# Kernel optimization log

Measured on AMD Instinct MI355X. Metric: run time of the kernel, lower is better.

## Reference

```python
import jax, jax.numpy as jnp
import numpy as np
import math

B, H, S, D = 4, 16, 4096, 128

def setup_inputs() -> dict:
    key = jax.random.key(0)
    kq, kk, kv = jax.random.split(key, 3)
    q = jax.random.normal(kq, (B, H, S, D), dtype=jnp.float32)
    k = jax.random.normal(kk, (B, H, S, D), dtype=jnp.float32)
    v = jax.random.normal(kv, (B, H, S, D), dtype=jnp.float32)
    return {"q": q, "k": k, "v": v}

def reference(q, k, v):
    # Faithful to the torch module: score = (q^T @ k) / sqrt(n_heads)
    # q^T contracts over the SEQUENCE axis -> (B, H, D, D) feature-attention.
    n_heads = q.shape[1]
    scale = 1.0 / math.sqrt(n_heads)
    score = jnp.einsum('bhsd,bhse->bhde', q, k) * scale  # (B,H,D,D)
    score = jax.nn.softmax(score, axis=-1)
    # score @ v^T -> (B,H,D,S)
    out = jnp.einsum('bhde,bhse->bhds', score, v)
    return out
```

## Files before the change

kernel.cpp:

```cpp
#include <hip/hip_runtime.h>

#define BH 64
#define S_ 4096
#define D_ 128
#define SCALE 0.25f

typedef __attribute__((ext_vector_type(4))) short short4v;
typedef __attribute__((ext_vector_type(8))) short short8v;
typedef __attribute__((ext_vector_type(4))) float f32x4;

__device__ inline unsigned short f2bf(float x) {
  union { float f; unsigned u; } v; v.f = x;
  unsigned r = v.u + 0x7fff + ((v.u >> 16) & 1);
  return (unsigned short)(r >> 16);
}
__device__ inline short8v cat8(short4v a, short4v b) {
  short8v r;
  r[0] = a[0]; r[1] = a[1]; r[2] = a[2]; r[3] = a[3];
  r[4] = b[0]; r[5] = b[1]; r[6] = b[2]; r[7] = b[3];
  return r;
}
__device__ inline short4v tr16(unsigned addr) {
  short4v r;
  asm volatile("ds_read_b64_tr_b16 %0, %1" : "=v"(r) : "v"(addr));
  return r;
}
__device__ inline void cvt_pair(float x0, float x1, unsigned& hi, unsigned& lo) {
  unsigned u0 = __float_as_uint(x0), u1 = __float_as_uint(x1);
  unsigned m0 = u0 & 0xffff0000u, m1 = u1 & 0xffff0000u;
  hi = m1 | (u0 >> 16);
  float l0 = x0 - __uint_as_float(m0);
  float l1 = x1 - __uint_as_float(m1);
  lo = (__float_as_uint(l1) & 0xffff0000u) | (__float_as_uint(l0) >> 16);
}

#define TILE_SH 4352
#define TILE_U  2176
#define TILE_B  (TILE_SH * 2)
#define BUF_SH  (4 * TILE_SH)
#define BUF_B   (4 * TILE_B)
#define ROW_B 272
#define ROW_U 68

template <int NKS, bool ATOMIC>
__global__ __launch_bounds__(512, 2) void qk_mfma(const float* __restrict__ q,
                                                  const float* __restrict__ k,
                                                  float* __restrict__ part) {
  constexpr int schunk = S_ / NKS;
  constexpr int nsteps = schunk / 32;
  static_assert(nsteps % 2 == 0, "nsteps must be even (buffer pairing)");
  const int bh = blockIdx.x;
  const int ks = blockIdx.y;
  const float* qb = q + (size_t)bh * S_ * D_ + (size_t)ks * schunk * D_;
  const float* kb = k + (size_t)bh * S_ * D_ + (size_t)ks * schunk * D_;

  __shared__ alignas(16) short lds[2 * BUF_SH];
  unsigned* ldsU0 = (unsigned*)&lds[0];
  unsigned* ldsU1 = (unsigned*)&lds[BUF_SH];
  const unsigned base_u = (unsigned)(uintptr_t)&lds[0];

  const int tid = threadIdx.x;
  const int wv = tid >> 6, lane = tid & 63;
  const int wm = wv & 3;
  const int wn = wv >> 2;

  f32x4 acc[2][4];
#pragma unroll
  for (int a = 0; a < 2; ++a)
#pragma unroll
    for (int b = 0; b < 4; ++b) acc[a][b] = (f32x4){0.f, 0.f, 0.f, 0.f};

  const int lrow = ((lane >> 4) << 2) + ((lane & 15) >> 2);
  const unsigned trbase = base_u + (unsigned)lrow * ROW_B + (unsigned)(lane & 3) * 8;
  const unsigned aQ0 = trbase;
  const unsigned aK0 = trbase + 2u * TILE_B;
  const unsigned aQ1 = aQ0 + BUF_B;
  const unsigned aK1 = aK0 + BUF_B;

  const int r0 = tid >> 5;
  const int r1 = (tid + 512) >> 5;
  const int c4 = tid & 31;

  float4 qr[2], kr[2];
  auto load_step = [&](int st) {
    size_t o0 = (size_t)(st * 32 + r0) * D_ + c4 * 4;
    size_t o1 = (size_t)(st * 32 + r1) * D_ + c4 * 4;
    qr[0] = *(const float4*)(qb + o0);
    qr[1] = *(const float4*)(qb + o1);
    kr[0] = *(const float4*)(kb + o0);
    kr[1] = *(const float4*)(kb + o1);
  };
  auto cvt_store = [&](unsigned* bufU) {
#pragma unroll
    for (int i = 0; i < 2; ++i) {
      int row = i ? r1 : r0;
      unsigned* p = bufU + row * ROW_U + c4 * 2;
      float4 xq = qr[i], xk = kr[i];
      unsigned h0, l0, h1, l1;
      cvt_pair(xq.x, xq.y, h0, l0);
      cvt_pair(xq.z, xq.w, h1, l1);
      *(uint2*)(p) = make_uint2(h0, h1);
      *(uint2*)(p + TILE_U) = make_uint2(l0, l1);
      cvt_pair(xk.x, xk.y, h0, l0);
      cvt_pair(xk.z, xk.w, h1, l1);
      *(uint2*)(p + 2 * TILE_U) = make_uint2(h0, h1);
      *(uint2*)(p + 3 * TILE_U) = make_uint2(l0, l1);
    }
  };

  auto iter = [&](int st, unsigned aQb, unsigned aKb, unsigned* stageU) {
    short4v Bf[4][2][2];
#pragma unroll
    for (int b = 0; b < 4; ++b) {
      unsigned cb = (unsigned)(wn * 4 + b) * 32;
#pragma unroll
      for (int ver = 0; ver < 2; ++ver)
#pragma unroll
        for (int kh = 0; kh < 2; ++kh)
          Bf[b][ver][kh] = tr16(aKb + ver * TILE_B + kh * (16 * ROW_B) + cb);
    }
    short4v Af[2][2][2];
#pragma unroll
    for (int a = 0; a < 2; ++a) {
      unsigned cb = (unsigned)(wm * 2 + a) * 32;
#pragma unroll
      for (int ver = 0; ver < 2; ++ver)
#pragma unroll
        for (int kh = 0; kh < 2; ++kh)
          Af[a][ver][kh] = tr16(aQb + ver * TILE_B + kh * (16 * ROW_B) + cb);
    }
    if (st + 1 < nsteps) cvt_store(stageU);
    if (st + 2 < nsteps) load_step(st + 2);
    asm volatile("s_waitcnt lgkmcnt(0)" ::: "memory");
    __builtin_amdgcn_sched_barrier(0);
#pragma unroll
    for (int a = 0; a < 2; ++a) {
      short8v ah = cat8(Af[a][0][0], Af[a][0][1]);
      short8v al = cat8(Af[a][1][0], Af[a][1][1]);
#pragma unroll
      for (int b = 0; b < 4; ++b) {
        short8v bh_ = cat8(Bf[b][0][0], Bf[b][0][1]);
        short8v bl_ = cat8(Bf[b][1][0], Bf[b][1][1]);
        acc[a][b] = __builtin_amdgcn_mfma_f32_16x16x32_bf16(ah, bh_, acc[a][b], 0, 0, 0);
        acc[a][b] = __builtin_amdgcn_mfma_f32_16x16x32_bf16(ah, bl_, acc[a][b], 0, 0, 0);
        acc[a][b] = __builtin_amdgcn_mfma_f32_16x16x32_bf16(al, bh_, acc[a][b], 0, 0, 0);
      }
    }
    __builtin_amdgcn_s_barrier();
  };

  load_step(0);
  cvt_store(ldsU0);
  if (nsteps > 1) load_step(1);
  asm volatile("s_waitcnt lgkmcnt(0)" ::: "memory");
  __builtin_amdgcn_s_barrier();

  for (int st = 0; st < nsteps; st += 2) {
    iter(st, aQ0, aK0, ldsU1);
    iter(st + 1, aQ1, aK1, ldsU0);
  }

  if (!ATOMIC) {
    float* dst = part + ((size_t)ks * BH + bh) * D_ * D_;
#pragma unroll
    for (int a = 0; a < 2; ++a)
#pragma unroll
      for (int b = 0; b < 4; ++b) {
        int e = (wn * 4 + b) * 16 + (lane & 15);
#pragma unroll
        for (int r = 0; r < 4; ++r) {
          int d = (wm * 2 + a) * 16 + ((lane >> 4) << 2) + r;
          dst[(size_t)d * D_ + e] = acc[a][b][r] * SCALE;
        }
      }
  } else {
    float* dst = part + (size_t)bh * D_ * D_;
#pragma unroll
    for (int a = 0; a < 2; ++a)
#pragma unroll
      for (int b = 0; b < 4; ++b) {
        int e = (wn * 4 + b) * 16 + (lane & 15);
#pragma unroll
        for (int r = 0; r < 4; ++r) {
          int d = (wm * 2 + a) * 16 + ((lane >> 4) << 2) + r;
          atomicAdd(&dst[(size_t)d * D_ + e], acc[a][b][r] * SCALE);
        }
      }
  }
}

template <int NKS>
__global__ __launch_bounds__(256) void softmax_k(const float* __restrict__ part,
                                                 short* __restrict__ Pg) {
  const int bh = blockIdx.x;
  const int wv = threadIdx.x >> 6, lane = threadIdx.x & 63;
  const size_t kstride = (size_t)BH * D_ * D_;
  const float* base = part + (size_t)bh * D_ * D_;
  short* dst = Pg + (size_t)bh * D_ * D_;
#pragma unroll
  for (int i = 0; i < 8; ++i) {
    int d = blockIdx.y * 32 + wv * 8 + i;
    float v0 = 0.f, v1 = 0.f;
    for (int ks2 = 0; ks2 < NKS; ++ks2) {
      const float* row = base + ks2 * kstride + (size_t)d * D_;
      v0 += row[lane];
      v1 += row[lane + 64];
    }
    float m = fmaxf(v0, v1);
#pragma unroll
    for (int off = 32; off; off >>= 1) m = fmaxf(m, __shfl_xor(m, off, 64));
    float e0 = __expf(v0 - m), e1 = __expf(v1 - m);
    float s = e0 + e1;
#pragma unroll
    for (int off = 32; off; off >>= 1) s += __shfl_xor(s, off, 64);
    float inv = 1.f / s;
    dst[(size_t)d * D_ + lane] = (short)f2bf(e0 * inv);
    dst[(size_t)d * D_ + lane + 64] = (short)f2bf(e1 * inv);
  }
}

__global__ __launch_bounds__(256) void pv_mfma(const short* __restrict__ Pg,
                                               const float* __restrict__ v,
                                               float* __restrict__ out) {
  const int bh = blockIdx.x;
  const int s0 = blockIdx.y * 128;
  const float* vb = v + (size_t)bh * S_ * D_;
  __shared__ alignas(16) short P_lds[128 * 136];
  __shared__ alignas(16) short V_lds[128 * 36];
  const int tid = threadIdx.x;
  const int wv = tid >> 6, lane = tid & 63;

  const short* Pb = Pg + (size_t)bh * D_ * D_;
#pragma unroll
  for (int i = 0; i < 8; ++i) {
    int idx8 = tid + i * 256;
    int row = idx8 >> 4, c8 = idx8 & 15;
    short8v val = *(const short8v*)(Pb + row * 128 + c8 * 8);
    *(short8v*)(P_lds + row * 136 + c8 * 8) = val;
  }

  f32x4 acc[8][2];
#pragma unroll
  for (int i = 0; i < 8; ++i)
#pragma unroll
    for (int j = 0; j < 2; ++j) acc[i][j] = (f32x4){0.f, 0.f, 0.f, 0.f};

#pragma unroll
  for (int es = 0; es < 4; ++es) {
    __syncthreads();
#pragma unroll
    for (int i = 0; i < 4; ++i) {
      int idx4 = tid + i * 256;
      int s = idx4 >> 3, c4 = idx4 & 7;
      float4 x = *(const float4*)(vb + (size_t)(s0 + s) * D_ + es * 32 + c4 * 4);
      short4v h;
      h[0] = (short)f2bf(x.x); h[1] = (short)f2bf(x.y);
      h[2] = (short)f2bf(x.z); h[3] = (short)f2bf(x.w);
      *(short4v*)(V_lds + s * 36 + c4 * 4) = h;
    }
    __syncthreads();

    short8v a[8];
#pragma unroll
    for (int mt = 0; mt < 8; ++mt) {
      int d = mt * 16 + (lane & 15);
      const short* pr = P_lds + d * 136 + es * 32 + ((lane >> 4) << 2);
      a[mt] = cat8(*(const short4v*)pr, *(const short4v*)(pr + 16));
    }
#pragma unroll
    for (int nl = 0; nl < 2; ++nl) {
      int srow = (wv * 2 + nl) * 16 + (lane & 15);
      const short* vr = V_lds + srow * 36 + ((lane >> 4) << 2);
      short8v b = cat8(*(const short4v*)vr, *(const short4v*)(vr + 16));
#pragma unroll
      for (int mt = 0; mt < 8; ++mt)
        acc[mt][nl] = __builtin_amdgcn_mfma_f32_16x16x32_bf16(a[mt], b, acc[mt][nl], 0, 0, 0);
    }
  }

  float* ob = out + (size_t)bh * D_ * S_ + s0;
#pragma unroll
  for (int mt = 0; mt < 8; ++mt)
#pragma unroll
    for (int nl = 0; nl < 2; ++nl) {
      int sc = (wv * 2 + nl) * 16 + (lane & 15);
#pragma unroll
      for (int r = 0; r < 4; ++r) {
        int d = mt * 16 + ((lane >> 4) << 2) + r;
        ob[(size_t)d * S_ + sc] = acc[mt][nl][r];
      }
    }
}

extern "C" void kernel_launch(void* const* d_in, const int* in_sizes, int n_in,
                              void* d_out, int out_size, void* d_ws,
                              size_t ws_size, hipStream_t stream) {
  const float* q = (const float*)d_in[0];
  const float* k = (const float*)d_in[1];
  const float* v = (const float*)d_in[2];
  float* out = (float*)d_out;
  char* ws = (char*)d_ws;

  const size_t PART1 = (size_t)BH * D_ * D_ * sizeof(float);
  const size_t PSZ = (size_t)BH * D_ * D_ * sizeof(short);

  if (ws_size >= 8 * PART1 + PSZ) {
    float* part = (float*)ws;
    short* Pg = (short*)(ws + 8 * PART1);
    qk_mfma<8, false><<<dim3(BH, 8), 512, 0, stream>>>(q, k, part);
    softmax_k<8><<<dim3(BH, 4), 256, 0, stream>>>(part, Pg);
    pv_mfma<<<dim3(BH, 32), 256, 0, stream>>>(Pg, v, out);
  } else {
    float* part = (float*)ws;
    short* Pg = (short*)(ws + PART1);
    hipMemsetAsync(ws, 0, PART1, stream);
    qk_mfma<16, true><<<dim3(BH, 16), 512, 0, stream>>>(q, k, part);
    softmax_k<1><<<dim3(BH, 4), 256, 0, stream>>>(part, Pg);
    pv_mfma<<<dim3(BH, 32), 256, 0, stream>>>(Pg, v, out);
  }
}
```

Baseline: 151.7 us.

## Store converted Q/K tiles in MFMA-blocked LDS layout without row padding

Replaces the padded row-major LDS tile layout (272-byte rows) with a blocked layout where each thread's converted values are written contiguously and the transpose-read addresses are computed from lane bit fields. Global loads are remapped so each thread fetches elements that land in the blocked order, which makes LDS stores fully linear and shrinks the LDS footprint. This aims to cut LDS bank conflicts and address arithmetic on the staging path, at the risk of less coalesced global loads and possible conflicts on the transposed reads.

Result: no change. 149.0 us (-1.7%).

```diff
diff --git a/kernel.cpp b/kernel.cpp
--- a/kernel.cpp
+++ b/kernel.cpp
@@ -34,13 +34,11 @@
   lo = (__float_as_uint(l1) & 0xffff0000u) | (__float_as_uint(l0) >> 16);
 }
 
-#define TILE_SH 4352
-#define TILE_U  2176
-#define TILE_B  (TILE_SH * 2)
-#define BUF_SH  (4 * TILE_SH)
-#define BUF_B   (4 * TILE_B)
-#define ROW_B 272
-#define ROW_U 68
+#define TILE_B2 8192
+#define TILE_U2 2048
+#define TILE_SH2 4096
+#define BUF_B2  (4 * TILE_B2)
+#define BUF_SH2 (4 * TILE_SH2)
 
 template <int NKS, bool ATOMIC>
 __global__ __launch_bounds__(512, 2) void qk_mfma(const float* __restrict__ q,
@@ -54,9 +52,9 @@
   const float* qb = q + (size_t)bh * S_ * D_ + (size_t)ks * schunk * D_;
   const float* kb = k + (size_t)bh * S_ * D_ + (size_t)ks * schunk * D_;
 
-  __shared__ alignas(16) short lds[2 * BUF_SH];
+  __shared__ alignas(16) short lds[2 * BUF_SH2];
   unsigned* ldsU0 = (unsigned*)&lds[0];
-  unsigned* ldsU1 = (unsigned*)&lds[BUF_SH];
+  unsigned* ldsU1 = (unsigned*)&lds[BUF_SH2];
   const unsigned base_u = (unsigned)(uintptr_t)&lds[0];
 
   const int tid = threadIdx.x;
@@ -70,21 +68,22 @@
 #pragma unroll
     for (int b = 0; b < 4; ++b) acc[a][b] = (f32x4){0.f, 0.f, 0.f, 0.f};
 
-  const int lrow = ((lane >> 4) << 2) + ((lane & 15) >> 2);
-  const unsigned trbase = base_u + (unsigned)lrow * ROW_B + (unsigned)(lane & 3) * 8;
+  const unsigned lconst = ((unsigned)(lane >> 4) << 10) |
+                          ((unsigned)((lane & 15) >> 2) << 5) |
+                          ((unsigned)(lane & 3) << 3);
+  const unsigned trbase = base_u + lconst;
   const unsigned aQ0 = trbase;
-  const unsigned aK0 = trbase + 2u * TILE_B;
-  const unsigned aQ1 = aQ0 + BUF_B;
-  const unsigned aK1 = aK0 + BUF_B;
-
-  const int r0 = tid >> 5;
-  const int r1 = (tid + 512) >> 5;
-  const int c4 = tid & 31;
+  const unsigned aK0 = trbase + 2u * TILE_B2;
+  const unsigned aQ1 = aQ0 + BUF_B2;
+  const unsigned aK1 = aK0 + BUF_B2;
+
+  const int row0 = ((tid >> 7) << 2) | ((tid >> 2) & 3);
+  const int col0 = (((tid >> 4) & 7) << 4) | ((tid & 3) << 2);
 
   float4 qr[2], kr[2];
   auto load_step = [&](int st) {
-    size_t o0 = (size_t)(st * 32 + r0) * D_ + c4 * 4;
-    size_t o1 = (size_t)(st * 32 + r1) * D_ + c4 * 4;
+    size_t o0 = (size_t)(st * 32 + row0) * D_ + col0;
+    size_t o1 = o0 + (size_t)16 * D_;
     qr[0] = *(const float4*)(qb + o0);
     qr[1] = *(const float4*)(qb + o1);
     kr[0] = *(const float4*)(kb + o0);
@@ -93,18 +92,16 @@
   auto cvt_store = [&](unsigned* bufU) {
 #pragma unroll
     for (int i = 0; i < 2; ++i) {
-      int row = i ? r1 : r0;
-      unsigned* p = bufU + row * ROW_U + c4 * 2;
-      float4 xq = qr[i], xk = kr[i];
+      unsigned off = (unsigned)(tid + i * 512) * 2;
       unsigned h0, l0, h1, l1;
-      cvt_pair(xq.x, xq.y, h0, l0);
-      cvt_pair(xq.z, xq.w, h1, l1);
-      *(uint2*)(p) = make_uint2(h0, h1);
-      *(uint2*)(p + TILE_U) = make_uint2(l0, l1);
-      cvt_pair(xk.x, xk.y, h0, l0);
-      cvt_pair(xk.z, xk.w, h1, l1);
-      *(uint2*)(p + 2 * TILE_U) = make_uint2(h0, h1);
-      *(uint2*)(p + 3 * TILE_U) = make_uint2(l0, l1);
+      cvt_pair(qr[i].x, qr[i].y, h0, l0);
+      cvt_pair(qr[i].z, qr[i].w, h1, l1);
+      *(uint2*)(bufU + off) = make_uint2(h0, h1);
+      *(uint2*)(bufU + TILE_U2 + off) = make_uint2(l0, l1);
+      cvt_pair(kr[i].x, kr[i].y, h0, l0);
+      cvt_pair(kr[i].z, kr[i].w, h1, l1);
+      *(uint2*)(bufU + 2 * TILE_U2 + off) = make_uint2(h0, h1);
+      *(uint2*)(bufU + 3 * TILE_U2 + off) = make_uint2(l0, l1);
     }
   };
 
@@ -112,22 +109,22 @@
     short4v Bf[4][2][2];
 #pragma unroll
     for (int b = 0; b < 4; ++b) {
-      unsigned cb = (unsigned)(wn * 4 + b) * 32;
+      unsigned cb = (unsigned)(wn * 4 + b) << 7;
 #pragma unroll
       for (int ver = 0; ver < 2; ++ver)
 #pragma unroll
         for (int kh = 0; kh < 2; ++kh)
-          Bf[b][ver][kh] = tr16(aKb + ver * TILE_B + kh * (16 * ROW_B) + cb);
+          Bf[b][ver][kh] = tr16(aKb + ver * TILE_B2 + kh * 4096 + cb);
     }
     short4v Af[2][2][2];
 #pragma unroll
     for (int a = 0; a < 2; ++a) {
-      unsigned cb = (unsigned)(wm * 2 + a) * 32;
+      unsigned cb = (unsigned)(wm * 2 + a) << 7;
 #pragma unroll
       for (int ver = 0; ver < 2; ++ver)
 #pragma unroll
         for (int kh = 0; kh < 2; ++kh)
-          Af[a][ver][kh] = tr16(aQb + ver * TILE_B + kh * (16 * ROW_B) + cb);
+          Af[a][ver][kh] = tr16(aQb + ver * TILE_B2 + kh * 4096 + cb);
     }
     if (st + 1 < nsteps) cvt_store(stageU);
     if (st + 2 < nsteps) load_step(st + 2);
```
